# Optimization experiments

Measured on AMD Instinct MI355X. Metric: run time of the kernel, lower is better.

## Reference

```python
import jax, jax.numpy as jnp
import numpy as np
from jax import lax

N = 16384          # num_nodes (LSTM sequence length, batch=1)
AVG_DEG = 32
E_EDGES = N * AVG_DEG
FEAT = 512         # cmd_args.feat_dim (tag vocab)
EMB = 256          # embedding_size -> LSTM input = 2*EMB
H = 512            # LSTM hidden_size
MLP_H = 512        # cmd_args.hidden
C = 10             # cmd_args.num_class


def setup_inputs() -> dict:
    key = jax.random.key(0)
    ks = jax.random.split(key, 14)
    s = 1.0 / np.sqrt(H)
    u = lambda k, shape: jax.random.uniform(k, shape, jnp.float32, -s, s)
    return {
        "node_tags": jax.random.randint(ks[0], (N,), 0, FEAT),
        "neighbor_node_ids": jax.random.randint(ks[1], (E_EDGES,), 0, N),
        "neighbor_tag_ids": jax.random.randint(ks[2], (E_EDGES,), 0, FEAT),
        "label": jax.random.randint(ks[3], (1,), 0, C),
        "W_emb": u(ks[4], (FEAT, EMB)),
        "b_emb": u(ks[5], (EMB,)),
        "W_ih": u(ks[6], (4 * H, 2 * EMB)),  # torch LSTM gate order: i, f, g, o
        "W_hh": u(ks[7], (4 * H, H)),
        "b_lstm": u(ks[8], (4 * H,)),        # b_ih + b_hh folded together
        "W1": u(ks[9], (H, MLP_H)),
        "b1": u(ks[10], (MLP_H,)),
        "W2": u(ks[11], (MLP_H, C)),
        "b2": u(ks[12], (C,)),
    }


def reference(node_tags, neighbor_node_ids, neighbor_tag_ids, label,
              W_emb, b_emb, W_ih, W_hh, b_lstm, W1, b1, W2, b2):
    n = node_tags.shape[0]
    feat_dim = W_emb.shape[0]
    hid = W_hh.shape[1]

    # one-hot(node_tags) @ W_emb + b  ==  row-gather of W_emb
    node_emb = W_emb[node_tags] + b_emb                      # [N, EMB]

    # ragged neighbor-tag histogram via scatter-add (the Python double loop)
    hist = jnp.zeros((n, feat_dim), dtype=W_emb.dtype)
    hist = hist.at[neighbor_node_ids, neighbor_tag_ids].add(1.0)  # [N, FEAT]
    nb_emb = hist @ W_emb + b_emb                            # [N, EMB]

    x = jnp.concatenate([node_emb, nb_emb], axis=1)          # [N, 2*EMB]

    # single-layer LSTM, batch=1, seq_len=N; precompute input projections
    pre = x @ W_ih.T + b_lstm                                # [N, 4H]

    def step(carry, p):
        h, c = carry
        g = p + h @ W_hh.T                                   # [4H]
        i, f, gg, o = jnp.split(g, 4)
        i = jax.nn.sigmoid(i)
        f = jax.nn.sigmoid(f)
        o = jax.nn.sigmoid(o)
        c = f * c + i * jnp.tanh(gg)
        h = o * jnp.tanh(c)
        return (h, c), h

    init = (jnp.zeros((hid,), x.dtype), jnp.zeros((hid,), x.dtype))
    _, hs = lax.scan(step, init, pre)                        # hs: [N, H]

    embed = jnp.sum(hs, axis=0)[None, :]                     # [1, H] (sum over time)

    # MLPClassifier: Linear -> ReLU -> Linear -> log_softmax
    h1 = jax.nn.relu(embed @ W1 + b1)
    logits = h1 @ W2 + b2                                    # [1, C]
    return jax.nn.log_softmax(logits, axis=-1)
```

## Files before the change

### kernel.cpp

```cpp
#include <hip/hip_runtime.h>
#include <hip/hip_bf16.h>

#define N_NODES 16384
#define E_EDGESN (16384*32)
#define FEAT 512
#define EMB 256
#define HID 512
#define G4 2048
#define XDIM 512
#define NWG 32
#define NLAUNCH 256
#define UPW 16
#define BLK 8

typedef __attribute__((ext_vector_type(8))) short bf16x8;
typedef __attribute__((ext_vector_type(4))) float f32x4;

__device__ __forceinline__ float b2f(unsigned short u) {
  union { unsigned int i; float f; } v; v.i = ((unsigned int)u) << 16; return v.f;
}
__device__ __forceinline__ unsigned short f2b(float f) {
  union { float f; unsigned int i; } v; v.f = f;
  unsigned int x = v.i;
  unsigned int r = (x + 0x7FFFu + ((x >> 16) & 1u)) >> 16;
  return (unsigned short)r;
}
__device__ __forceinline__ float fast_sigmoid(float x) {
  return __builtin_amdgcn_rcpf(1.0f + __expf(-x));
}
__device__ __forceinline__ float fast_tanh(float x) {
  return fmaf(-2.0f, __builtin_amdgcn_rcpf(1.0f + __expf(2.0f * x)), 1.0f);
}

__global__ __launch_bounds__(256) void k_detect(const unsigned* __restrict__ w,
                                                unsigned* __restrict__ flag) {
  __shared__ int cnt;
  if (threadIdx.x == 0) cnt = 0;
  __syncthreads();
  int hits = 0;
#pragma unroll
  for (int j = 0; j < 4; ++j) {
    unsigned wv = w[threadIdx.x * 4 + j];
    unsigned e = (wv >> 7) & 0xFFu;
    if ((e >= 90u && e <= 126u) || ((wv & 0xFFFFu) == 0u)) hits++;
  }
  atomicAdd(&cnt, hits);
  __syncthreads();
  if (threadIdx.x == 0) *flag = (cnt < 512) ? 1u : 0u;
}

__global__ void k_convert(const void* __restrict__ src, unsigned short* __restrict__ dst,
                          int n, const unsigned* __restrict__ flag) {
  int i = blockIdx.x * blockDim.x + threadIdx.x;
  if (i >= n) return;
  if (*flag) dst[i] = f2b(((const float*)src)[i]);
  else       dst[i] = ((const unsigned short*)src)[i];
}

__global__ void k_hist(const int* __restrict__ nid, const int* __restrict__ ntag,
                       unsigned* __restrict__ hist) {
  int e = blockIdx.x * blockDim.x + threadIdx.x;
  if (e < E_EDGESN)
    atomicAdd(&hist[(size_t)nid[e] * FEAT + ntag[e]], 1u);
}

__global__ __launch_bounds__(256) void k_build_x(
    const int* __restrict__ tags, const unsigned* __restrict__ hist,
    const unsigned short* __restrict__ Wemb, const unsigned short* __restrict__ bemb,
    unsigned short* __restrict__ x) {
  __shared__ int f_lds[160];
  __shared__ float c_lds[160];
  __shared__ int nlist;
  int n = blockIdx.x, c = threadIdx.x;
  if (c == 0) nlist = 0;
  __syncthreads();
  for (int f = c; f < FEAT; f += 256) {
    unsigned cnt = hist[(size_t)n * FEAT + f];
    if (cnt) {
      int idx = atomicAdd(&nlist, 1);
      if (idx < 160) { f_lds[idx] = f; c_lds[idx] = (float)cnt; }
    }
  }
  __syncthreads();
  int m = nlist; if (m > 160) m = 160;
  float be = b2f(bemb[c]);
  int tg = tags[n];
  x[(size_t)n * XDIM + c] = f2b(b2f(Wemb[(size_t)tg * EMB + c]) + be);
  float acc = be;
  for (int j = 0; j < m; ++j)
    acc += c_lds[j] * b2f(Wemb[(size_t)f_lds[j] * EMB + c]);
  x[(size_t)n * XDIM + EMB + c] = f2b(acc);
}

__global__ __launch_bounds__(256) void k_gemm_pre(
    const unsigned short* __restrict__ x, const unsigned short* __restrict__ Wih,
    const unsigned short* __restrict__ blstm, unsigned short* __restrict__ pre) {
  int wave = threadIdx.x >> 6, lane = threadIdx.x & 63;
  int row = lane & 15, quad = lane >> 4;
  int mband = blockIdx.y * 64 + wave * 16;
  int nbase = blockIdx.x * 128;
  f32x4 acc[8] = {};
  const unsigned short* ap = x + (size_t)(mband + row) * XDIM + quad * 8;
  const unsigned short* bp0 = Wih + (size_t)(nbase + row) * XDIM + quad * 8;
  for (int kc = 0; kc < 16; ++kc) {
    bf16x8 af = *(const bf16x8*)(ap + kc * 32);
#pragma unroll
    for (int nt = 0; nt < 8; ++nt) {
      bf16x8 bf = *(const bf16x8*)(bp0 + (size_t)nt * 16 * XDIM + kc * 32);
      acc[nt] = __builtin_amdgcn_mfma_f32_16x16x32_bf16(af, bf, acc[nt], 0, 0, 0);
    }
  }
#pragma unroll
  for (int nt = 0; nt < 8; ++nt) {
    int nn = nbase + nt * 16 + row;
    float bv = b2f(blstm[nn]);
    int pn = ((nn & 511) << 2) | (nn >> 9);
#pragma unroll
    for (int i = 0; i < 4; ++i) {
      int mm = mband + quad * 4 + i;
      pre[(size_t)mm * G4 + pn] = f2b(acc[nt][i] + bv);
    }
  }
}

__global__ __launch_bounds__(256, 1) void k_scan(
    const unsigned short* __restrict__ Whh, const unsigned short* __restrict__ prep,
    unsigned* __restrict__ hwF, unsigned* __restrict__ hwS,
    float* __restrict__ embed, int* __restrict__ elect) {
  __shared__ float h_lds[HID];
  __shared__ int rank_s;
  int tid = threadIdx.x;

  if (tid == 0) {
    unsigned xcd;
    asm volatile("s_getreg_b32 %0, hwreg(HW_REG_XCC_ID)" : "=s"(xcd));
    xcd &= 7u;
    int idx = atomicAdd(&elect[xcd], 1);
    int rank = -1;
    if (idx < NWG) {
      if (idx == NWG - 1) atomicCAS(&elect[8], -1, (int)xcd);
      int w;
      while ((w = __hip_atomic_load(&elect[8], __ATOMIC_RELAXED,
                                    __HIP_MEMORY_SCOPE_AGENT)) == -1)
        __builtin_amdgcn_s_sleep(8);
      if (w == (int)xcd) rank = idx;
    }
    rank_s = rank;
  }
  __syncthreads();
  int wg = rank_s;
  if (wg < 0) return;

  int ug = tid >> 4;
  int s  = tid & 15;
  int unit = wg * UPW + ug;

  float wreg[4][32];
#pragma unroll
  for (int g = 0; g < 4; ++g) {
    const unsigned* wp = (const unsigned*)(Whh + (size_t)(g * HID + unit) * HID);
#pragma unroll
    for (int j = 0; j < 16; ++j) {
      unsigned wv = wp[16 * j + s];
      wreg[g][2 * j]     = b2f((unsigned short)(wv & 0xFFFFu));
      wreg[g][2 * j + 1] = b2f((unsigned short)(wv >> 16));
    }
  }

  ushort4 pcblk[BLK];
  if (s == 0) {
#pragma unroll
    for (int i = 0; i < BLK; ++i)
      pcblk[i] = *(const ushort4*)(prep + (size_t)i * G4 + (unsigned)unit * 4u);
  }

  float cstate = 0.0f, eacc = 0.0f;
  h_lds[tid] = 0.0f;
  h_lds[256 + tid] = 0.0f;
  __syncthreads();

  unsigned long long fB = (unsigned long long)hwF;
  unsigned long long sB = (unsigned long long)hwS;
  int pollslow = 0;
  int stepfails = 0;

  for (int tb = 0; tb < N_NODES; tb += BLK) {
#pragma unroll
    for (int p = 0; p < BLK; ++p) {
      int t = tb + p;
      float a0 = 0.f, a1 = 0.f, a2 = 0.f, a3 = 0.f;
      const float2* hb = (const float2*)h_lds;
#pragma unroll
      for (int j = 0; j < 16; ++j) {
        float2 hv = hb[j * 16 + s];
        a0 += wreg[0][2*j] * hv.x + wreg[0][2*j+1] * hv.y;
        a1 += wreg[1][2*j] * hv.x + wreg[1][2*j+1] * hv.y;
        a2 += wreg[2][2*j] * hv.x + wreg[2][2*j+1] * hv.y;
        a3 += wreg[3][2*j] * hv.x + wreg[3][2*j+1] * hv.y;
      }
#pragma unroll
      for (int off = 1; off < 16; off <<= 1) {
        a0 += __shfl_xor(a0, off);
        a1 += __shfl_xor(a1, off);
        a2 += __shfl_xor(a2, off);
        a3 += __shfl_xor(a3, off);
      }

      unsigned tagw = (unsigned)t & 0xFFFFu;
      unsigned slotoff = (unsigned)((t & 1) << 12);

      if (s == 0) {
        float gi = fast_sigmoid(a0 + b2f(pcblk[p].x));
        float gf = fast_sigmoid(a1 + b2f(pcblk[p].y));
        float gg = fast_tanh   (a2 + b2f(pcblk[p].z));
        float go = fast_sigmoid(a3 + b2f(pcblk[p].w));
        cstate = gf * cstate + gi * gg;
        float hn = go * fast_tanh(cstate);
        eacc += hn;
        if (t < N_NODES - 1) {
          union { float f; unsigned u; } cu; cu.f = hn;
          unsigned long long sv =
              (((unsigned long long)((cu.u << 16) | tagw)) << 32) |
              (unsigned long long)((cu.u & 0xFFFF0000u) | tagw);
          unsigned long long saF = fB + slotoff + (unsigned)unit * 8u;
          asm volatile("global_store_dwordx2 %0, %1, off"
                       :: "v"(saF), "v"(sv) : "memory");
          __hip_atomic_store((unsigned long long*)(uintptr_t)(sB + slotoff + (unsigned)unit * 8u),
                             sv, __ATOMIC_RELAXED, __HIP_MEMORY_SCOPE_AGENT);
        }
        if (p == BLK - 1) {
#pragma unroll
          for (int i = 0; i < BLK; ++i) {
            int row = tb + BLK + i;
            if (row >= N_NODES) row = 0;
            pcblk[i] = *(const ushort4*)(prep + (size_t)row * G4 + (unsigned)unit * 4u);
          }
        }
      }

      if (t < N_NODES - 1) {
        unsigned long long pa = fB + slotoff + (unsigned)tid * 16u;
        unsigned long long qa = sB + slotoff + (unsigned)tid * 16u;
        unsigned v0, v1, v2, v3;
        int got = 0;
        if (!pollslow) {
          for (int tries = 0; tries < 64; ++tries) {
            unsigned long long a, b;
            asm volatile("global_load_dwordx2 %0, %2, off sc0\n\t"
                         "global_load_dwordx2 %1, %3, off sc0\n\t"
                         "s_waitcnt vmcnt(0)"
                         : "=v"(a), "=v"(b) : "v"(pa), "v"(pa + 8u) : "memory");
            v0 = (unsigned)a; v1 = (unsigned)(a >> 32);
            v2 = (unsigned)b; v3 = (unsigned)(b >> 32);
            if ((((v0 ^ tagw) | (v1 ^ tagw) | (v2 ^ tagw) | (v3 ^ tagw)) & 0xFFFFu) == 0u) {
              got = 1; break;
            }
          }
          if (!got && ++stepfails >= 12) pollslow = 1;
        }
        if (!got) {
          unsigned long long* q0 = (unsigned long long*)(uintptr_t)qa;
          unsigned long long* q1 = (unsigned long long*)(uintptr_t)(qa + 8u);
          for (;;) {
            unsigned long long a = __hip_atomic_load(q0, __ATOMIC_RELAXED, __HIP_MEMORY_SCOPE_AGENT);
            unsigned long long b = __hip_atomic_load(q1, __ATOMIC_RELAXED, __HIP_MEMORY_SCOPE_AGENT);
            v0 = (unsigned)a; v1 = (unsigned)(a >> 32);
            v2 = (unsigned)b; v3 = (unsigned)(b >> 32);
            if ((((v0 ^ tagw) | (v1 ^ tagw) | (v2 ^ tagw) | (v3 ^ tagw)) & 0xFFFFu) == 0u) break;
            __builtin_amdgcn_s_sleep(1);
          }
        }
        union { unsigned u; float f; } r0, r1;
        r0.u = (v0 & 0xFFFF0000u) | (v1 >> 16);
        r1.u = (v2 & 0xFFFF0000u) | (v3 >> 16);
        h_lds[2 * tid]     = r0.f;
        h_lds[2 * tid + 1] = r1.f;
        __syncthreads();
      }
    }
  }
  if (s == 0) embed[unit] = eacc;
}

__global__ __launch_bounds__(512) void k_head(
    const float* __restrict__ embed, const unsigned short* __restrict__ W1,
    const unsigned short* __restrict__ b1, const unsigned short* __restrict__ W2,
    const unsigned short* __restrict__ b2, void* __restrict__ out,
    const unsigned* __restrict__ flag) {
  __shared__ float e_s[HID], h1_s[HID];
  __shared__ float lg[16];
  int tid = threadIdx.x;
  e_s[tid] = embed[tid];
  __syncthreads();
  float sum = b2f(b1[tid]);
  for (int i = 0; i < HID; ++i)
    sum += e_s[i] * b2f(W1[(size_t)i * HID + tid]);
  h1_s[tid] = fmaxf(sum, 0.0f);
  __syncthreads();
  if (tid < 10) {
    float l = b2f(b2[tid]);
    for (int j = 0; j < HID; ++j)
      l += h1_s[j] * b2f(W2[(size_t)j * 10 + tid]);
    lg[tid] = l;
  }
  __syncthreads();
  if (tid == 0) {
    float m = -1e30f;
    for (int c = 0; c < 10; ++c) m = fmaxf(m, lg[c]);
    float se = 0.f;
    for (int c = 0; c < 10; ++c) se += expf(lg[c] - m);
    float lse = m + logf(se);
    if (*flag) {
      for (int c = 0; c < 10; ++c) ((float*)out)[c] = lg[c] - lse;
    } else {
      for (int c = 0; c < 10; ++c) ((unsigned short*)out)[c] = f2b(lg[c] - lse);
    }
  }
}

extern "C" void kernel_launch(void* const* d_in, const int* in_sizes, int n_in,
                              void* d_out, int out_size, void* d_ws, size_t ws_size,
                              hipStream_t stream) {
  const int* node_tags = (const int*)d_in[0];
  const int* nid = (const int*)d_in[1];
  const int* ntag = (const int*)d_in[2];

  char* ws = (char*)d_ws;
  unsigned short* pre  = (unsigned short*)ws;
  unsigned short* x    = (unsigned short*)(ws + 67108864);
  unsigned*       hist = (unsigned*)(ws + 83886080);
  char* tail = ws + 117440512;
  unsigned* hwF   = (unsigned*)tail;
  unsigned* hwS   = (unsigned*)(tail + 8192);
  unsigned* flag  = (unsigned*)(tail + 16384);
  float*    embed = (float*)(tail + 16448);
  int*      elect = (int*)(tail + 18496);
  char* wc = tail + 20480;
  unsigned short* Wemb_c  = (unsigned short*)(wc);
  unsigned short* bemb_c  = (unsigned short*)(wc + 262144);
  unsigned short* Wih_c   = (unsigned short*)(wc + 262656);
  unsigned short* Whh_c   = (unsigned short*)(wc + 2359808);
  unsigned short* blstm_c = (unsigned short*)(wc + 4456960);
  unsigned short* W1_c    = (unsigned short*)(wc + 4461056);
  unsigned short* b1_c    = (unsigned short*)(wc + 4985344);
  unsigned short* W2_c    = (unsigned short*)(wc + 4986368);
  unsigned short* b2_c    = (unsigned short*)(wc + 4996608);

  hipMemsetAsync(hist, 0, 33554432, stream);
  hipMemsetAsync(elect, 0, 32, stream);
  hipMemsetAsync(elect + 8, 0xFF, 4, stream);

  k_detect<<<1, 256, 0, stream>>>((const unsigned*)d_in[6], flag);

  struct { const void* s; unsigned short* d; int n; } cv[9] = {
    { d_in[4],  Wemb_c,  FEAT * EMB },
    { d_in[5],  bemb_c,  EMB },
    { d_in[6],  Wih_c,   G4 * XDIM },
    { d_in[7],  Whh_c,   G4 * HID },
    { d_in[8],  blstm_c, G4 },
    { d_in[9],  W1_c,    HID * HID },
    { d_in[10], b1_c,    HID },
    { d_in[11], W2_c,    HID * 10 },
    { d_in[12], b2_c,    10 },
  };
  for (int i = 0; i < 9; ++i)
    k_convert<<<(cv[i].n + 255) / 256, 256, 0, stream>>>(cv[i].s, cv[i].d, cv[i].n, flag);

  k_hist<<<E_EDGESN / 256, 256, 0, stream>>>(nid, ntag, hist);
  k_build_x<<<N_NODES, 256, 0, stream>>>(node_tags, hist, Wemb_c, bemb_c, x);
  k_gemm_pre<<<dim3(G4 / 128, N_NODES / 64), 256, 0, stream>>>(x, Wih_c, blstm_c, pre);
  k_scan<<<NLAUNCH, 256, 0, stream>>>(Whh_c, pre, hwF, hwS, embed, elect);
  k_head<<<1, 512, 0, stream>>>(embed, W1_c, b1_c, W2_c, b2_c, d_out, flag);
}
```

Baseline: 32.64 ms.

## Poll hidden-state slots with atomics and split fast/slow publishes across lanes

The fast-path poll of the exchanged hidden-state slots now uses atomic OR-with-zero returns instead of sc0 loads, and the fast-slot publish becomes an atomic swap. Two lanes per unit now compute the gate nonlinearity redundantly, so the fast-slot and slow-slot stores are issued by different lanes in parallel. Preactivations are held by lane 4 and broadcast with shuffles. The preactivation prefetch block grows from 8 to 16 and the poll retry limits are lowered. Atomics should see remote writes sooner through L2, but they cost more per poll and the larger prefetch block adds register pressure.

```diff
diff --git a/kernel.cpp b/kernel.cpp
--- a/kernel.cpp
+++ b/kernel.cpp
@@ -11,7 +11,7 @@
 #define NWG 32
 #define NLAUNCH 256
 #define UPW 16
-#define BLK 8
+#define BLK 16
 
 typedef __attribute__((ext_vector_type(8))) short bf16x8;
 typedef __attribute__((ext_vector_type(4))) float f32x4;
@@ -153,6 +153,7 @@
 
   int ug = tid >> 4;
   int s  = tid & 15;
+  int lane = tid & 63;
   int unit = wg * UPW + ug;
 
   float wreg[4][32];
@@ -167,11 +168,13 @@
     }
   }
 
-  ushort4 pcblk[BLK];
-  if (s == 0) {
-#pragma unroll
-    for (int i = 0; i < BLK; ++i)
-      pcblk[i] = *(const ushort4*)(prep + (size_t)i * G4 + (unsigned)unit * 4u);
+  unsigned pc0[BLK], pc1[BLK];
+  if (s == 4) {
+#pragma unroll
+    for (int i = 0; i < BLK; ++i) {
+      const unsigned* pp = (const unsigned*)(prep + (size_t)i * G4 + (unsigned)unit * 4u);
+      pc0[i] = pp[0]; pc1[i] = pp[1];
+    }
   }
 
   float cstate = 0.0f, eacc = 0.0f;
@@ -181,8 +184,10 @@
 
   unsigned long long fB = (unsigned long long)hwF;
   unsigned long long sB = (unsigned long long)hwS;
+  unsigned long long zero64 = 0ULL;
   int pollslow = 0;
   int stepfails = 0;
+  int bsrc = (lane & 48) | 4;
 
   for (int tb = 0; tb < N_NODES; tb += BLK) {
 #pragma unroll
@@ -206,35 +211,42 @@
         a3 += __shfl_xor(a3, off);
       }
 
+      unsigned w0 = __shfl(pc0[p], bsrc, 64);
+      unsigned w1 = __shfl(pc1[p], bsrc, 64);
+
       unsigned tagw = (unsigned)t & 0xFFFFu;
       unsigned slotoff = (unsigned)((t & 1) << 12);
 
-      if (s == 0) {
-        float gi = fast_sigmoid(a0 + b2f(pcblk[p].x));
-        float gf = fast_sigmoid(a1 + b2f(pcblk[p].y));
-        float gg = fast_tanh   (a2 + b2f(pcblk[p].z));
-        float go = fast_sigmoid(a3 + b2f(pcblk[p].w));
+      if ((s & 7) == 0) {
+        float gi = fast_sigmoid(a0 + b2f((unsigned short)(w0 & 0xFFFFu)));
+        float gf = fast_sigmoid(a1 + b2f((unsigned short)(w0 >> 16)));
+        float gg = fast_tanh   (a2 + b2f((unsigned short)(w1 & 0xFFFFu)));
+        float go = fast_sigmoid(a3 + b2f((unsigned short)(w1 >> 16)));
         cstate = gf * cstate + gi * gg;
         float hn = go * fast_tanh(cstate);
-        eacc += hn;
+        if (s == 0) eacc += hn;
         if (t < N_NODES - 1) {
           union { float f; unsigned u; } cu; cu.f = hn;
           unsigned long long sv =
               (((unsigned long long)((cu.u << 16) | tagw)) << 32) |
               (unsigned long long)((cu.u & 0xFFFF0000u) | tagw);
-          unsigned long long saF = fB + slotoff + (unsigned)unit * 8u;
-          asm volatile("global_store_dwordx2 %0, %1, off"
-                       :: "v"(saF), "v"(sv) : "memory");
-          __hip_atomic_store((unsigned long long*)(uintptr_t)(sB + slotoff + (unsigned)unit * 8u),
-                             sv, __ATOMIC_RELAXED, __HIP_MEMORY_SCOPE_AGENT);
+          if (s == 0) {
+            unsigned long long saF = fB + slotoff + (unsigned)unit * 8u;
+            asm volatile("global_atomic_swap_x2 %0, %1, off"
+                         :: "v"(saF), "v"(sv) : "memory");
+          } else {
+            __hip_atomic_store((unsigned long long*)(uintptr_t)(sB + slotoff + (unsigned)unit * 8u),
+                               sv, __ATOMIC_RELAXED, __HIP_MEMORY_SCOPE_AGENT);
+          }
         }
-        if (p == BLK - 1) {
-#pragma unroll
-          for (int i = 0; i < BLK; ++i) {
-            int row = tb + BLK + i;
-            if (row >= N_NODES) row = 0;
-            pcblk[i] = *(const ushort4*)(prep + (size_t)row * G4 + (unsigned)unit * 4u);
-          }
+      }
+      if (s == 4 && p == BLK - 1) {
+#pragma unroll
+        for (int i = 0; i < BLK; ++i) {
+          int row = tb + BLK + i;
+          if (row >= N_NODES) row = 0;
+          const unsigned* pp = (const unsigned*)(prep + (size_t)row * G4 + (unsigned)unit * 4u);
+          pc0[i] = pp[0]; pc1[i] = pp[1];
         }
       }
 
@@ -244,19 +256,21 @@
         unsigned v0, v1, v2, v3;
         int got = 0;
         if (!pollslow) {
-          for (int tries = 0; tries < 64; ++tries) {
+          for (int tries = 0; tries < 48; ++tries) {
             unsigned long long a, b;
-            asm volatile("global_load_dwordx2 %0, %2, off sc0\n\t"
-                         "global_load_dwordx2 %1, %3, off sc0\n\t"
+            asm volatile("global_atomic_or_x2 %0, %2, %4, off sc0\n\t"
+                         "global_atomic_or_x2 %1, %3, %4, off sc0\n\t"
                          "s_waitcnt vmcnt(0)"
-                         : "=v"(a), "=v"(b) : "v"(pa), "v"(pa + 8u) : "memory");
+                         : "=&v"(a), "=&v"(b)
+                         : "v"(pa), "v"(pa + 8u), "v"(zero64)
+                         : "memory");
             v0 = (unsigned)a; v1 = (unsigned)(a >> 32);
             v2 = (unsigned)b; v3 = (unsigned)(b >> 32);
             if ((((v0 ^ tagw) | (v1 ^ tagw) | (v2 ^ tagw) | (v3 ^ tagw)) & 0xFFFFu) == 0u) {
               got = 1; break;
             }
           }
-          if (!got && ++stepfails >= 12) pollslow = 1;
+          if (!got && ++stepfails >= 8) pollslow = 1;
         }
         if (!got) {
           unsigned long long* q0 = (unsigned long long*)(uintptr_t)qa;
```

New measurement: 60.72 ms. 1.86x slower.
